# Kernel optimization log

Hardware: AMD Instinct MI355X
Metric: run time of the kernel (lower is better)

The kernel has to match this reference:

```python
import jax, jax.numpy as jnp
import numpy as np

N, L, S = 512, 1024, 32   # batch, latent dim, spatial (S*S == L)
F = 32 * S * S            # flattened encoder conv features (last conv = 32 ch)
H = 512                   # hidden width of latent MLP heads


def _lrelu(x):
    return jnp.where(x >= 0, x, 0.01 * x)


def _bn(x):
    # BatchNorm2d in training mode, gamma=1, beta=0 (default init)
    m = x.mean((0, 2, 3), keepdims=True)
    v = x.var((0, 2, 3), keepdims=True)
    return (x - m) * jax.lax.rsqrt(v + 1e-5)


def _conv(x, w, b):
    y = jax.lax.conv_general_dilated(x, w, (1, 1), 'SAME',
                                     dimension_numbers=('NCHW', 'OIHW', 'NCHW'))
    return y + b[None, :, None, None]


def _block(x, w, b):
    return _lrelu(_bn(_conv(x, w, b)))


def setup_inputs() -> dict:
    key = jax.random.key(0)
    ks = jax.random.split(key, 16)
    r = lambda k, s, sc: jax.random.normal(k, s, jnp.float32) * sc
    return {
        'x': r(ks[0], (N, 1, S, S), 1.0),
        'eps_c': r(ks[1], (N, L), 1.0),
        'eps_s': r(ks[2], (N, L), 1.0),
        'enc_cw1': r(ks[3], (2, 32, 1, 3, 3), 0.1),   'enc_cb1': jnp.zeros((2, 32)),
        'enc_cw2': r(ks[4], (2, 64, 32, 3, 3), 0.05), 'enc_cb2': jnp.zeros((2, 64)),
        'enc_cw3': r(ks[5], (2, 32, 64, 3, 3), 0.05), 'enc_cb3': jnp.zeros((2, 32)),
        'enc_muW1': r(ks[6], (2, H, F), 0.005), 'enc_muB1': jnp.zeros((2, H)),
        'enc_muW2': r(ks[7], (2, L, H), 0.02),  'enc_muB2': jnp.zeros((2, L)),
        'enc_vaW1': r(ks[8], (2, H, F), 0.005), 'enc_vaB1': jnp.zeros((2, H)),
        'enc_vaW2': r(ks[9], (2, L, H), 0.02),  'enc_vaB2': jnp.zeros((2, L)),
        'dec_cw1': r(ks[10], (2, 32, 1, 3, 3), 0.1),   'dec_cb1': jnp.zeros((2, 32)),
        'dec_cw2': r(ks[11], (2, 64, 32, 3, 3), 0.05), 'dec_cb2': jnp.zeros((2, 64)),
        'dec_cw3': r(ks[12], (2, 1, 64, 3, 3), 0.05),  'dec_cb3': jnp.zeros((2, 1)),
    }


def reference(x, eps_c, eps_s,
              enc_cw1, enc_cb1, enc_cw2, enc_cb2, enc_cw3, enc_cb3,
              enc_muW1, enc_muB1, enc_muW2, enc_muB2,
              enc_vaW1, enc_vaB1, enc_vaW2, enc_vaB2,
              dec_cw1, dec_cb1, dec_cw2, dec_cb2, dec_cw3, dec_cb3):
    def encode(i):
        h = _block(x, enc_cw1[i], enc_cb1[i])
        h = _block(h, enc_cw2[i], enc_cb2[i])
        h = _block(h, enc_cw3[i], enc_cb3[i])
        f = h.reshape(N, -1)                                   # [N, F]
        mu = _lrelu(_lrelu(f @ enc_muW1[i].T + enc_muB1[i]) @ enc_muW2[i].T + enc_muB2[i])
        lv = _lrelu(_lrelu(f @ enc_vaW1[i].T + enc_vaB1[i]) @ enc_vaW2[i].T + enc_vaB2[i])
        return mu, lv                                          # each [N, L]

    def decode(z, i):
        h = z.reshape(N, 1, S, S)
        h = _block(h, dec_cw1[i], dec_cb1[i])
        h = _block(h, dec_cw2[i], dec_cb2[i])
        h = _block(h, dec_cw3[i], dec_cb3[i])
        return h.reshape(N, 1, S, S)

    class_mu, class_logvar = encode(0)
    style_mu, style_logvar = encode(1)

    # precision-weighted product-of-experts group evidence (vectorized)
    precision = jnp.exp(-style_logvar)                  # 1/var, [N, L]
    group_var = 1.0 / precision.sum(0)                  # [L]
    group_mu = (style_mu * precision).sum(0) * group_var  # [L]
    group_logvar = jnp.log(group_var)

    # reparameterize
    z_c = eps_c * jnp.exp(0.5 * class_logvar) + class_mu          # [N, L]
    z_s = eps_s * jnp.exp(0.5 * group_logvar)[None] + group_mu[None]  # [N, L]

    output_c = decode(z_c, 0)
    output_s = jax.nn.relu(decode(z_s, 1))
    output = output_c * output_s                        # [N, 1, S, S]

    kl1 = -0.5 * jnp.sum(1.0 + class_logvar) + 0.5 * (
        jnp.sum(class_mu ** 2) + jnp.sum(jnp.exp(class_logvar) ** 2))
    kl2 = -0.5 * jnp.sum(1.0 + group_logvar) + 0.5 * (
        jnp.sum(group_mu ** 2) + jnp.sum(jnp.exp(group_logvar) ** 2))
    recon = (jnp.exp(x) - jnp.exp(output)) ** 2
    loss = -kl1 + kl2 + recon                           # [N, 1, S, S]
    return loss, output
```

## Files before the change

### kernel.cpp

```cpp
#include <hip/hip_runtime.h>

constexpr int N_   = 512;
constexpr int PIX  = 1024;
constexpr int L_   = 1024;
constexpr int F_   = 32768;
constexpr int H_   = 512;
constexpr float IC_ = 1.0f / (float)(512 * 1024);

__device__ __forceinline__ float lrelu(float t) { return t >= 0.f ? t : 0.01f * t; }

using frag  = __attribute__((ext_vector_type(8))) short;
using f32x4 = __attribute__((ext_vector_type(4))) float;
using s4    = __attribute__((ext_vector_type(4))) short;

#define BAR() do {                                              \
    asm volatile("s_waitcnt lgkmcnt(0)" ::: "memory");          \
    __builtin_amdgcn_s_barrier();                               \
    asm volatile("" ::: "memory");                              \
} while (0)

__device__ __forceinline__ void split_bf16(float v, short& hi, short& lo) {
    const unsigned b = __float_as_uint(v);
    hi = (short)(b >> 16);
    const float hf = __uint_as_float(b & 0xFFFF0000u);
    lo = (short)(__float_as_uint(v - hf) >> 16);
}

__device__ __forceinline__ frag ld2(const short* p) {
    union { frag f; struct { unsigned long long a, b; } u; } x;
    x.u.a = *(const unsigned long long*)(p);
    x.u.b = *(const unsigned long long*)(p + 4);
    return x.f;
}

__global__ __launch_bounds__(256) void wsplit6_kernel(
    const float* __restrict__ w0, const float* __restrict__ w1,
    const float* __restrict__ w2, const float* __restrict__ w3,
    const float* __restrict__ w4, const float* __restrict__ w5,
    short* __restrict__ hi, short* __restrict__ lo)
{
    const int layer = blockIdx.y;
    const float* W = layer == 0 ? w0 : layer == 1 ? w1 : layer == 2 ? w2 :
                     layer == 3 ? w3 : layer == 4 ? w4 : w5;
    const int CIN  = (layer == 1 || layer == 3) ? 64 : 32;
    const int NCOT = (layer == 1 || layer == 3) ? 2 : 4;
    const int idx = blockIdx.x * 256 + threadIdx.x;
    const int j    = idx & 7;
    const int lane = (idx >> 3) & 63;
    const int q    = lane >> 4, lm = lane & 15;
    const int blk  = idx >> 9;
    const int cot  = blk % NCOT;
    const int rest = blk / NCOT;
    const int pos  = rest % 9;
    const int cc   = rest / 9;
    const int co = cot * 16 + lm;
    const int ci = cc * 32 + q * 8 + j;
    short h, l;
    split_bf16(W[((size_t)co * CIN + ci) * 9 + pos], h, l);
    hi[layer * 18432 + idx] = h;
    lo[layer * 18432 + idx] = l;
}

template<int CIN, int COUT, bool BN_IN>
__global__ __launch_bounds__(512) void conv_mfma(
    const float* __restrict__ in, const short* __restrict__ wh,
    const short* __restrict__ wl, const float* __restrict__ bias,
    float* __restrict__ out, const float* __restrict__ stats_in,
    float* __restrict__ stats_out)
{
    constexpr int NCOT  = COUT / 16;
    constexpr int NCOT2 = NCOT / 2;
    constexpr int NCH   = CIN / 32;
    constexpr int STR  = 36;
    constexpr int PLsh = 340 * STR;
    __shared__ __align__(16) short hiL[PLsh];
    __shared__ __align__(16) short loL[PLsh];
    __shared__ float red[2 * COUT];
    __shared__ float bnm[64], bni[64];
    const int tid  = threadIdx.x;
    const int n    = blockIdx.x >> 2;
    const int y0   = (blockIdx.x & 3) << 3;
    const int lane = tid & 63;
    const int wv   = tid >> 6;
    const int pgrp = wv & 3;
    const int cotg = wv >> 2;
    const int lm   = lane & 15;
    const int q    = lane >> 4;

    if (tid < 2 * COUT) red[tid] = 0.f;
    if (BN_IN && tid < CIN) {
        const float m  = stats_in[tid] * IC_;
        const float qq = stats_in[CIN + tid] * IC_;
        bnm[tid] = m;
        bni[tid] = rsqrtf(qq - m * m + 1e-5f);
    }
    __syncthreads();

    f32x4 acc[NCOT2][4];
#pragma unroll
    for (int t = 0; t < NCOT2; ++t)
#pragma unroll
        for (int pt = 0; pt < 4; ++pt) acc[t][pt] = {0.f, 0.f, 0.f, 0.f};

    const int rs0 = tid / 34, cs0 = tid % 34;
    const int gr0 = y0 - 1 + rs0, gc0 = cs0 - 1;
    const bool act = tid < 340;
    const bool ok0 = act && ((unsigned)gr0 < 32u) && ((unsigned)gc0 < 32u);
    const int  po0 = gr0 * 32 + gc0;

    const float* inb = in + ((size_t)n * CIN << 10);

    frag ahA[NCOT2], alA[NCOT2], ahB[NCOT2], alB[NCOT2];

    auto LDW = [&](frag (&dh)[NCOT2], frag (&dl)[NCOT2], int posAbs) {
#pragma unroll
        for (int t = 0; t < NCOT2; ++t) {
            const int cot = cotg * NCOT2 + t;
            const size_t wb = (size_t)((posAbs * NCOT + cot) * 512 + lane * 8);
            dh[t] = *(const frag*)&wh[wb];
            dl[t] = *(const frag*)&wl[wb];
        }
    };

    auto COMPUTE = [&](int pos, frag (&fh)[NCOT2], frag (&fl)[NCOT2]) {
        const int ky = pos / 3, kx = pos - ky * 3;
        __builtin_amdgcn_s_setprio(1);
#pragma unroll
        for (int pt = 0; pt < 4; ++pt) {
            const int ptile = pgrp * 4 + pt;
            const int row = ptile >> 1;
            const int col = ((ptile & 1) << 4) + lm;
            const int loff = ((row + ky) * 34 + col + kx) * STR + q * 8;
            const frag bh = ld2(&hiL[loff]);
            const frag bl = ld2(&loL[loff]);
#pragma unroll
            for (int t = 0; t < NCOT2; ++t) {
                acc[t][pt] = __builtin_amdgcn_mfma_f32_16x16x32_bf16(
                    fh[t], bh, acc[t][pt], 0, 0, 0);
                acc[t][pt] = __builtin_amdgcn_mfma_f32_16x16x32_bf16(
                    fh[t], bl, acc[t][pt], 0, 0, 0);
                acc[t][pt] = __builtin_amdgcn_mfma_f32_16x16x32_bf16(
                    fl[t], bh, acc[t][pt], 0, 0, 0);
            }
        }
        __builtin_amdgcn_s_setprio(0);
    };

#pragma unroll 1
    for (int cc = 0; cc < NCH; ++cc) {
        if (cc) BAR();

        LDW(ahA, alA, cc * 9 + 0);

#pragma unroll 1
        for (int cb = 0; cb < 32; cb += 16) {
            float v0r[16];
#pragma unroll
            for (int u = 0; u < 16; ++u) {
                const int cg = cc * 32 + cb + u;
                v0r[u] = ok0 ? inb[((size_t)cg << 10) + po0] : 0.f;
            }
            if (act) {
#pragma unroll
                for (int u4 = 0; u4 < 16; u4 += 4) {
                    s4 h0v, l0v;
#pragma unroll
                    for (int e = 0; e < 4; ++e) {
                        const int ci = cb + u4 + e;
                        const int cg = cc * 32 + ci;
                        float v0 = v0r[u4 + e];
                        if (BN_IN && ok0) v0 = lrelu((v0 - bnm[cg]) * bni[cg]);
                        short h, l;
                        split_bf16(v0, h, l);
                        h0v[e] = h; l0v[e] = l;
                    }
                    *(s4*)&hiL[tid * STR + cb + u4] = h0v;
                    *(s4*)&loL[tid * STR + cb + u4] = l0v;
                }
            }
        }
        BAR();

#pragma unroll 1
        for (int pos = 0; pos < 8; pos += 2) {
            LDW(ahB, alB, cc * 9 + pos + 1);
            COMPUTE(pos, ahA, alA);
            LDW(ahA, alA, cc * 9 + pos + 2);
            COMPUTE(pos + 1, ahB, alB);
        }
        COMPUTE(8, ahA, alA);
    }

    float* ob = out + ((size_t)n * COUT << 10);
#pragma unroll
    for (int t = 0; t < NCOT2; ++t) {
#pragma unroll
        for (int r = 0; r < 4; ++r) {
            const int co = (cotg * NCOT2 + t) * 16 + q * 4 + r;
            const float b = bias[co];
            float s = 0.f, sq = 0.f;
#pragma unroll
            for (int pt = 0; pt < 4; ++pt) {
                const int ptile = pgrp * 4 + pt;
                const float v = acc[t][pt][r] + b;
                ob[((size_t)co << 10) + (y0 << 5) + (ptile << 4) + lm] = v;
                s += v; sq += v * v;
            }
#pragma unroll
            for (int off = 8; off > 0; off >>= 1) {
                s  += __shfl_down(s, off, 64);
                sq += __shfl_down(sq, off, 64);
            }
            if (lm == 0) {
                atomicAdd(&red[co], s);
                atomicAdd(&red[COUT + co], sq);
            }
        }
    }
    __syncthreads();
    if (tid < 2 * COUT) atomicAdd(&stats_out[tid], red[tid]);
}

template<int CIN, int COPB, bool BN_IN>
__global__ __launch_bounds__(256) void conv3x3(
    const float* __restrict__ in, const float* __restrict__ w,
    const float* __restrict__ bias, float* __restrict__ out,
    const float* __restrict__ stats_in, float* __restrict__ stats_out,
    int Cout)
{
    constexpr int CT = (CIN < 4) ? CIN : 4;
    __shared__ float tile[CT * PIX];
    __shared__ float red[2 * COPB];
    const int groups = Cout / COPB;
    const int n   = blockIdx.x / groups;
    const int co0 = (blockIdx.x % groups) * COPB;
    const int tid = threadIdx.x;
    const int x   = tid & 31;
    const int y0  = (tid >> 5) * 4;

    float acc[COPB][4];
#pragma unroll
    for (int c = 0; c < COPB; ++c)
#pragma unroll
        for (int j = 0; j < 4; ++j) acc[c][j] = 0.f;

    const float* inbase = in + (size_t)n * CIN * PIX;

#pragma unroll 1
    for (int s0 = 0; s0 < CIN; s0 += CT) {
        __syncthreads();
#pragma unroll
        for (int s = 0; s < CT; ++s) {
            float4 v = ((const float4*)(inbase + (size_t)(s0 + s) * PIX))[tid];
            if (BN_IN) {
                const int c = s0 + s;
                const float m   = stats_in[c] * IC_;
                const float q   = stats_in[CIN + c] * IC_;
                const float inv = rsqrtf(q - m * m + 1e-5f);
                v.x = lrelu((v.x - m) * inv);
                v.y = lrelu((v.y - m) * inv);
                v.z = lrelu((v.z - m) * inv);
                v.w = lrelu((v.w - m) * inv);
            }
            ((float4*)tile)[s * 256 + tid] = v;
        }
        __syncthreads();
#pragma unroll 2
        for (int s = 0; s < CT; ++s) {
            const int ci = s0 + s;
            const float* tp = tile + s * PIX;
            float r[6][3];
#pragma unroll
            for (int ry = 0; ry < 6; ++ry) {
                const int yy = y0 + ry - 1;
                const bool yok = (unsigned)yy < 32u;
#pragma unroll
                for (int cx = 0; cx < 3; ++cx) {
                    const int xx = x + cx - 1;
                    const bool ok = yok && ((unsigned)xx < 32u);
                    r[ry][cx] = ok ? tp[yy * 32 + xx] : 0.f;
                }
            }
#pragma unroll
            for (int c = 0; c < COPB; ++c) {
                const float* wp = w + ((size_t)(co0 + c) * CIN + ci) * 9;
#pragma unroll
                for (int ky = 0; ky < 3; ++ky)
#pragma unroll
                    for (int kx = 0; kx < 3; ++kx) {
                        const float wv = wp[ky * 3 + kx];
#pragma unroll
                        for (int j = 0; j < 4; ++j)
                            acc[c][j] += r[ky + j][kx] * wv;
                    }
            }
        }
    }

    if (tid < 2 * COPB) red[tid] = 0.f;
    __syncthreads();
#pragma unroll
    for (int c = 0; c < COPB; ++c) {
        const float b = bias[co0 + c];
        float* ob = out + (((size_t)n * Cout + co0 + c) << 10);
        float s = 0.f, q = 0.f;
#pragma unroll
        for (int j = 0; j < 4; ++j) {
            const float v = acc[c][j] + b;
            ob[(y0 + j) * 32 + x] = v;
            s += v; q += v * v;
        }
#pragma unroll
        for (int off = 32; off > 0; off >>= 1) {
            s += __shfl_down(s, off, 64);
            q += __shfl_down(q, off, 64);
        }
        if ((tid & 63) == 0) {
            atomicAdd(&red[c], s);
            atomicAdd(&red[COPB + c], q);
        }
    }
    __syncthreads();
    if (tid < COPB)
        atomicAdd(&stats_out[co0 + tid], red[tid]);
    else if (tid < 2 * COPB)
        atomicAdd(&stats_out[Cout + co0 + tid - COPB], red[tid]);
}

template<int MODE>
__global__ __launch_bounds__(256) void gemm_mfma(
    const float* __restrict__ A0, const float* __restrict__ A1,
    const float* __restrict__ B0, const float* __restrict__ B1,
    float* __restrict__ C0, float* __restrict__ C1,
    int K, int Nh, int kchunk, int xph,
    const float* __restrict__ bnstats, int Cin,
    const float* __restrict__ ba0, const float* __restrict__ ba1)
{
    __shared__ short AhL[8192], AlL[8192], BhL[8192], BlL[8192];
    const int tid  = threadIdx.x;
    const int head = blockIdx.x / xph;
    const int n0   = (blockIdx.x % xph) * 128;
    const int m0   = blockIdx.y * 128;
    const float* A = head ? A1 : A0;
    const float* B = head ? B1 : B0;
    float*       C = head ? C1 : C0;
    const float* BA = head ? ba1 : ba0;
    const int k0 = blockIdx.z * kchunk;

    const int lane = tid & 63;
    const int wv   = tid >> 6;
    const int wm   = wv & 1;
    const int wn   = wv >> 1;
    const int lm   = lane & 15;
    const int q    = lane >> 4;

    const int srow = tid >> 1;
    const int smt  = srow >> 4;
    const int slm  = srow & 15;
    const int sq0  = (tid & 1) * 2;
    const int ks   = (tid & 1) * 16;

    float bnm0 = 0.f, bni0 = 1.f, bnm1 = 0.f, bni1 = 1.f;
    if (MODE == 1) {
        const int c0 = k0 >> 10;
        bnm0 = bnstats[c0] * IC_;
        const float q0 = bnstats[Cin + c0] * IC_;
        bni0 = rsqrtf(q0 - bnm0 * bnm0 + 1e-5f);
        const int c1 = (c0 + 1 < Cin) ? c0 + 1 : c0;
        bnm1 = bnstats[c1] * IC_;
        const float q1 = bnstats[Cin + c1] * IC_;
        bni1 = rsqrtf(q1 - bnm1 * bnm1 + 1e-5f);
    }

    f32x4 acc[4][4];
#pragma unroll
    for (int i = 0; i < 4; ++i)
#pragma unroll
        for (int j = 0; j < 4; ++j) acc[i][j] = {0.f, 0.f, 0.f, 0.f};

    auto cv8 = [](float4 u, float4 w2, frag& h, frag& l) {
        const float v[8] = {u.x, u.y, u.z, u.w, w2.x, w2.y, w2.z, w2.w};
#pragma unroll
        for (int e = 0; e < 8; ++e) {
            short hh, ll;
            split_bf16(v[e], hh, ll);
            h[e] = hh; l[e] = ll;
        }
    };

    float4 a4[4], b4[4];
    auto LOADAB = [&](int kb) {
        const float* Ap = A + (size_t)(m0 + srow) * K + kb + ks;
        const float* Bp = B + (size_t)(n0 + srow) * K + kb + ks;
#pragma unroll
        for (int g = 0; g < 4; ++g) a4[g] = ((const float4*)Ap)[g];
#pragma unroll
        for (int g = 0; g < 4; ++g) b4[g] = ((const float4*)Bp)[g];
    };

    const int o0 = ((smt * 4 + sq0) * 16 + slm) * 8;
    const int o1 = ((smt * 4 + sq0 + 1) * 16 + slm) * 8;

    auto STAGE = [&](int s) {
        if (MODE == 1) {
            const int sel = s >> 5;
            const float m   = sel ? bnm1 : bnm0;
            const float inv = sel ? bni1 : bni0;
#pragma unroll
            for (int g = 0; g < 4; ++g) {
                a4[g].x = lrelu((a4[g].x - m) * inv);
                a4[g].y = lrelu((a4[g].y - m) * inv);
                a4[g].z = lrelu((a4[g].z - m) * inv);
                a4[g].w = lrelu((a4[g].w - m) * inv);
            }
        }
        if (MODE == 2) {
            const float* bp = BA + k0 + s * 32 + ks;
#pragma unroll
            for (int g = 0; g < 4; ++g) {
                const float4 bv = ((const float4*)bp)[g];
                a4[g].x = lrelu(a4[g].x + bv.x);
                a4[g].y = lrelu(a4[g].y + bv.y);
                a4[g].z = lrelu(a4[g].z + bv.z);
                a4[g].w = lrelu(a4[g].w + bv.w);
            }
        }
        frag ah0, al0, ah1, al1, bh0, bl0, bh1, bl1;
        cv8(a4[0], a4[1], ah0, al0);
        cv8(a4[2], a4[3], ah1, al1);
        cv8(b4[0], b4[1], bh0, bl0);
        cv8(b4[2], b4[3], bh1, bl1);
        const int pb = (s & 1) << 12;
        *(frag*)&AhL[pb + o0] = ah0;  *(frag*)&AhL[pb + o1] = ah1;
        *(frag*)&AlL[pb + o0] = al0;  *(frag*)&AlL[pb + o1] = al1;
        *(frag*)&BhL[pb + o0] = bh0;  *(frag*)&BhL[pb + o1] = bh1;
        *(frag*)&BlL[pb + o0] = bl0;  *(frag*)&BlL[pb + o1] = bl1;
    };

    auto MMA = [&](int s) {
        const int pb = (s & 1) << 12;
        frag fah[4], fal[4], fbh[4], fbl[4];
#pragma unroll
        for (int t = 0; t < 4; ++t) {
            const int oa = pb + (((wm * 4 + t) * 4 + q) * 16 + lm) * 8;
            const int ob = pb + (((wn * 4 + t) * 4 + q) * 16 + lm) * 8;
            fah[t] = *(const frag*)&AhL[oa];
            fal[t] = *(const frag*)&AlL[oa];
            fbh[t] = *(const frag*)&BhL[ob];
            fbl[t] = *(const frag*)&BlL[ob];
        }
        __builtin_amdgcn_s_setprio(1);
#pragma unroll
        for (int i = 0; i < 4; ++i)
#pragma unroll
            for (int j = 0; j < 4; ++j) {
                acc[i][j] = __builtin_amdgcn_mfma_f32_16x16x32_bf16(
                    fah[i], fbh[j], acc[i][j], 0, 0, 0);
                acc[i][j] = __builtin_amdgcn_mfma_f32_16x16x32_bf16(
                    fah[i], fbl[j], acc[i][j], 0, 0, 0);
                acc[i][j] = __builtin_amdgcn_mfma_f32_16x16x32_bf16(
                    fal[i], fbh[j], acc[i][j], 0, 0, 0);
            }
        __builtin_amdgcn_s_setprio(0);
    };

    const int T = kchunk >> 5;

    LOADAB(k0);
    STAGE(0);
    LOADAB(k0 + 32);
    BAR();

#pragma unroll 1
    for (int s = 1; s < T; ++s) {
        MMA(s - 1);
        STAGE(s);
        if (s + 1 < T) LOADAB(k0 + (s + 1) * 32);
        BAR();
    }
    MMA(T - 1);

#pragma unroll
    for (int i = 0; i < 4; ++i) {
        const int m = m0 + wm * 64 + i * 16 + q * 4;
#pragma unroll
        for (int j = 0; j < 4; ++j) {
            const int n = n0 + wn * 64 + j * 16 + lm;
            float* cp = C + (size_t)m * Nh + n;
#pragma unroll
            for (int r = 0; r < 4; ++r)
                atomicAdd(cp + (size_t)r * Nh, acc[i][j][r]);
        }
    }
}

__device__ __forceinline__ void block_reduce_atomic(float t, float* target)
{
#pragma unroll
    for (int off = 32; off > 0; off >>= 1) t += __shfl_down(t, off, 64);
    __shared__ float lt[4];
    const int wave = threadIdx.x >> 6, lane = threadIdx.x & 63;
    if (lane == 0) lt[wave] = t;
    __syncthreads();
    if (threadIdx.x == 0) atomicAdd(target, lt[0] + lt[1] + lt[2] + lt[3]);
}

__global__ __launch_bounds__(256) void poe_kernel(
    const float* __restrict__ mu1, const float* __restrict__ lv1,
    const float* __restrict__ bmu, const float* __restrict__ blv,
    float* __restrict__ gmu, float* __restrict__ glv, float* __restrict__ kl)
{
    const int l = blockIdx.x * 256 + threadIdx.x;
    const float bm = bmu[l], bl = blv[l];
    float sp = 0.f, sm = 0.f;
    for (int n = 0; n < N_; ++n) {
        const float lv = lrelu(lv1[(size_t)n * L_ + l] + bl);
        const float p  = expf(-lv);
        sp += p;
        sm += lrelu(mu1[(size_t)n * L_ + l] + bm) * p;
    }
    const float gv = 1.f / sp;
    const float gm = sm * gv;
    const float gl = -logf(sp);
    gmu[l] = gm;
    glv[l] = gl;
    const float t = -0.5f * (1.f + gl) + 0.5f * (gm * gm + gv * gv);
    block_reduce_atomic(t, &kl[1]);
}

__global__ __launch_bounds__(256) void reparam_kernel(
    const float* __restrict__ mu0, const float* __restrict__ lv0,
    const float* __restrict__ bmu, const float* __restrict__ blv,
    const float* __restrict__ eps_c, const float* __restrict__ eps_s,
    const float* __restrict__ gmu, const float* __restrict__ glv,
    float* __restrict__ zc, float* __restrict__ zs, float* __restrict__ kl)
{
    const int idx = blockIdx.x * 256 + threadIdx.x;
    const int l = idx & (L_ - 1);
    const float m  = lrelu(mu0[idx] + bmu[l]);
    const float lv = lrelu(lv0[idx] + blv[l]);
    zc[idx] = eps_c[idx] * expf(0.5f * lv) + m;
    zs[idx] = eps_s[idx] * expf(0.5f * glv[l]) + gmu[l];
    const float e = expf(lv);
    const float t = -0.5f * (1.f + lv) + 0.5f * (m * m + e * e);
    block_reduce_atomic(t, &kl[0]);
}

__global__ __launch_bounds__(256) void final_kernel(
    const float* __restrict__ x, const float* __restrict__ oc,
    const float* __restrict__ os, const float* __restrict__ stC,
    const float* __restrict__ stS, const float* __restrict__ kl,
    float* __restrict__ out)
{
    const int idx = blockIdx.x * 256 + threadIdx.x;
    const float mc = stC[0] * IC_, qc = stC[1] * IC_;
    const float ivc = rsqrtf(qc - mc * mc + 1e-5f);
    const float ms = stS[0] * IC_, qs = stS[1] * IC_;
    const float ivs = rsqrtf(qs - ms * ms + 1e-5f);
    const float tc = lrelu((oc[idx] - mc) * ivc);
    const float ts = fmaxf((os[idx] - ms) * ivs, 0.f);
    const float o = tc * ts;
    const float d = expf(x[idx]) - expf(o);
    out[idx]            = -kl[0] + kl[1] + d * d;
    out[N_ * PIX + idx] = o;
}

extern "C" void kernel_launch(void* const* d_in, const int* in_sizes, int n_in,
                              void* d_out, int out_size, void* d_ws, size_t ws_size,
                              hipStream_t stream)
{
    const float* x        = (const float*)d_in[0];
    const float* eps_c    = (const float*)d_in[1];
    const float* eps_s    = (const float*)d_in[2];
    const float* enc_cw1  = (const float*)d_in[3];
    const float* enc_cb1  = (const float*)d_in[4];
    const float* enc_cw2  = (const float*)d_in[5];
    const float* enc_cb2  = (const float*)d_in[6];
    const float* enc_cw3  = (const float*)d_in[7];
    const float* enc_cb3  = (const float*)d_in[8];
    const float* enc_muW1 = (const float*)d_in[9];
    const float* enc_muB1 = (const float*)d_in[10];
    const float* enc_muW2 = (const float*)d_in[11];
    const float* enc_muB2 = (const float*)d_in[12];
    const float* enc_vaW1 = (const float*)d_in[13];
    const float* enc_vaB1 = (const float*)d_in[14];
    const float* enc_vaW2 = (const float*)d_in[15];
    const float* enc_vaB2 = (const float*)d_in[16];
    const float* dec_cw1  = (const float*)d_in[17];
    const float* dec_cb1  = (const float*)d_in[18];
    const float* dec_cw2  = (const float*)d_in[19];
    const float* dec_cb2  = (const float*)d_in[20];
    const float* dec_cw3  = (const float*)d_in[21];
    const float* dec_cb3  = (const float*)d_in[22];
    float* out = (float*)d_out;

    float* ws   = (float*)d_ws;
    float* bufA = ws;
    float* bufB = bufA + (size_t)N_ * 64 * PIX;
    float* h1   = bufB + (size_t)N_ * 32 * PIX;
    float* h2   = h1 + N_ * H_;
    float* mu0  = h2 + N_ * H_;
    float* lv0  = mu0 + N_ * L_;
    float* mu1  = lv0 + N_ * L_;
    float* lv1  = mu1 + N_ * L_;
    float* zc   = lv1 + N_ * L_;
    float* zs   = zc + N_ * L_;
    float* oc   = zs + N_ * L_;
    float* os   = oc + N_ * L_;
    float* gmu  = os + N_ * L_;
    float* glv  = gmu + L_;
    float* stats = glv + L_;
    float* kl   = stats + 12 * 128;
    short* wsh  = (short*)(kl + 4);
    short* wsl  = wsh + 6 * 18432;

    auto st  = [&](int s) { return stats + 128 * s; };
    auto whp = [&](int layer) { return wsh + layer * 18432; };
    auto wlp = [&](int layer) { return wsl + layer * 18432; };

    hipMemsetAsync(stats, 0, (12 * 128 + 4) * sizeof(float), stream);

    wsplit6_kernel<<<dim3(72, 6), 256, 0, stream>>>(
        enc_cw2, enc_cw3, enc_cw2 + 64 * 32 * 9, enc_cw3 + 32 * 64 * 9,
        dec_cw2, dec_cw2 + 64 * 32 * 9, wsh, wsl);

    for (int i = 0; i < 2; ++i) {
        const float* cw1 = enc_cw1 + (size_t)i * 32 * 9;
        const float* cb1 = enc_cb1 + (size_t)i * 32;
        const float* cb2 = enc_cb2 + (size_t)i * 64;
        const float* cb3 = enc_cb3 + (size_t)i * 32;

        conv3x3<1, 16, false><<<N_ * 2, 256, 0, stream>>>(
            x, cw1, cb1, bufB, nullptr, st(i * 3 + 0), 32);
        conv_mfma<32, 64, true><<<N_ * 4, 512, 0, stream>>>(
            bufB, whp(i * 2), wlp(i * 2), cb2, bufA, st(i * 3 + 0), st(i * 3 + 1));
        conv_mfma<64, 32, true><<<N_ * 4, 512, 0, stream>>>(
            bufA, whp(i * 2 + 1), wlp(i * 2 + 1), cb3, bufB, st(i * 3 + 1), st(i * 3 + 2));

        const float* W1m = enc_muW1 + (size_t)i * H_ * F_;
        const float* B1m = enc_muB1 + (size_t)i * H_;
        const float* W2m = enc_muW2 + (size_t)i * L_ * H_;
        const float* W1v = enc_vaW1 + (size_t)i * H_ * F_;
        const float* B1v = enc_vaB1 + (size_t)i * H_;
        const float* W2v = enc_vaW2 + (size_t)i * L_ * H_;
        float* mu_i = (i == 0) ? mu0 : mu1;
        float* lv_i = (i == 0) ? lv0 : lv1;

        hipMemsetAsync(h1, 0, (size_t)2 * N_ * H_ * sizeof(float), stream);
        gemm_mfma<1><<<dim3(8, 4, 16), 256, 0, stream>>>(
            bufB, bufB, W1m, W1v, h1, h2, F_, H_, 2048, 4,
            st(i * 3 + 2), 32, nullptr, nullptr);

        hipMemsetAsync(mu_i, 0, (size_t)2 * N_ * L_ * sizeof(float), stream);
        gemm_mfma<2><<<dim3(16, 4, 4), 256, 0, stream>>>(
            h1, h2, W2m, W2v, mu_i, lv_i, H_, L_, 128, 8,
            nullptr, 0, B1m, B1v);
    }

    poe_kernel<<<L_ / 256, 256, 0, stream>>>(
        mu1, lv1, enc_muB2 + L_, enc_vaB2 + L_, gmu, glv, kl);
    reparam_kernel<<<(N_ * L_) / 256, 256, 0, stream>>>(
        mu0, lv0, enc_muB2, enc_vaB2, eps_c, eps_s, gmu, glv, zc, zs, kl);

    for (int i = 0; i < 2; ++i) {
        const float* cw1 = dec_cw1 + (size_t)i * 32 * 9;
        const float* cb1 = dec_cb1 + (size_t)i * 32;
        const float* cb2 = dec_cb2 + (size_t)i * 64;
        const float* cw3 = dec_cw3 + (size_t)i * 64 * 9;
        const float* cb3 = dec_cb3 + (size_t)i * 1;
        const float* zi = (i == 0) ? zc : zs;
        float* oi = (i == 0) ? oc : os;

        conv3x3<1, 16, false><<<N_ * 2, 256, 0, stream>>>(
            zi, cw1, cb1, bufB, nullptr, st(6 + i * 3 + 0), 32);
        conv_mfma<32, 64, true><<<N_ * 4, 512, 0, stream>>>(
            bufB, whp(4 + i), wlp(4 + i), cb2, bufA, st(6 + i * 3 + 0), st(6 + i * 3 + 1));
        conv3x3<64, 1, true><<<N_, 256, 0, stream>>>(
            bufA, cw3, cb3, oi, st(6 + i * 3 + 1), st(6 + i * 3 + 2), 1);
    }

    final_kernel<<<(N_ * PIX) / 256, 256, 0, stream>>>(
        x, oc, os, st(8), st(11), kl, out);
}
```

Measured before the change: 1.365 ms.

## Load GEMM tiles straight to LDS as fp32 and split to bf16 after reading

The MFMA GEMM now fills double-buffered fp32 LDS tiles with global_load_lds (16-byte, XOR-swizzled) instead of loading through registers and writing pre-split bf16 hi/lo tiles. The BN/bias activation and the bf16 hi/lo split move into the MMA stage, applied to fragments read from LDS. The aim is to cut register staging and VALU work between the global loads and the LDS stores, and to overlap the next tile's loads with the current tile's MFMAs. In exchange, conversion now sits on the critical path before the MFMAs, and there is a full vmcnt wait plus a barrier every stage.

```diff
diff --git a/kernel.cpp b/kernel.cpp
--- a/kernel.cpp
+++ b/kernel.cpp
@@ -31,6 +31,12 @@
     x.u.a = *(const unsigned long long*)(p);
     x.u.b = *(const unsigned long long*)(p + 4);
     return x.f;
+}
+
+__device__ __forceinline__ void gll16(const float* g, float* l) {
+    __builtin_amdgcn_global_load_lds(
+        (const __attribute__((address_space(1))) void*)g,
+        (__attribute__((address_space(3))) void*)l, 16, 0, 0);
 }
 
 __global__ __launch_bounds__(256) void wsplit6_kernel(
@@ -336,7 +342,8 @@
     const float* __restrict__ bnstats, int Cin,
     const float* __restrict__ ba0, const float* __restrict__ ba1)
 {
-    __shared__ short AhL[8192], AlL[8192], BhL[8192], BlL[8192];
+    __shared__ __align__(16) float AfL[2 * 4096];
+    __shared__ __align__(16) float BfL[2 * 4096];
     const int tid  = threadIdx.x;
     const int head = blockIdx.x / xph;
     const int n0   = (blockIdx.x % xph) * 128;
@@ -354,11 +361,8 @@
     const int lm   = lane & 15;
     const int q    = lane >> 4;
 
-    const int srow = tid >> 1;
-    const int smt  = srow >> 4;
-    const int slm  = srow & 15;
-    const int sq0  = (tid & 1) * 2;
-    const int ks   = (tid & 1) * 16;
+    const int lrow = lane >> 3;
+    const int lpk  = ((lane & 7) ^ lrow) << 2;
 
     float bnm0 = 0.f, bni0 = 1.f, bnm1 = 0.f, bni1 = 1.f;
     if (MODE == 1) {
@@ -378,76 +382,56 @@
 #pragma unroll
         for (int j = 0; j < 4; ++j) acc[i][j] = {0.f, 0.f, 0.f, 0.f};
 
-    auto cv8 = [](float4 u, float4 w2, frag& h, frag& l) {
-        const float v[8] = {u.x, u.y, u.z, u.w, w2.x, w2.y, w2.z, w2.w};
-#pragma unroll
-        for (int e = 0; e < 8; ++e) {
-            short hh, ll;
-            split_bf16(v[e], hh, ll);
-            h[e] = hh; l[e] = ll;
+    auto ISSUE = [&](int s, int kb) {
+        float* lba = &AfL[(s & 1) << 12];
+        float* lbb = &BfL[(s & 1) << 12];
+#pragma unroll
+        for (int j = 0; j < 4; ++j) {
+            const int c = wv * 4 + j;
+            const int row = (c << 3) + lrow;
+            gll16(A + (size_t)(m0 + row) * K + kb + lpk, lba + (c << 8));
+            gll16(B + (size_t)(n0 + row) * K + kb + lpk, lbb + (c << 8));
         }
     };
 
-    float4 a4[4], b4[4];
-    auto LOADAB = [&](int kb) {
-        const float* Ap = A + (size_t)(m0 + srow) * K + kb + ks;
-        const float* Bp = B + (size_t)(n0 + srow) * K + kb + ks;
-#pragma unroll
-        for (int g = 0; g < 4; ++g) a4[g] = ((const float4*)Ap)[g];
-#pragma unroll
-        for (int g = 0; g < 4; ++g) b4[g] = ((const float4*)Bp)[g];
-    };
-
-    const int o0 = ((smt * 4 + sq0) * 16 + slm) * 8;
-    const int o1 = ((smt * 4 + sq0 + 1) * 16 + slm) * 8;
-
-    auto STAGE = [&](int s) {
+    auto MMA = [&](int s, int kb) {
+        const float* Ap = &AfL[(s & 1) << 12];
+        const float* Bp = &BfL[(s & 1) << 12];
+        float bm = 0.f, bi = 1.f;
         if (MODE == 1) {
-            const int sel = s >> 5;
-            const float m   = sel ? bnm1 : bnm0;
-            const float inv = sel ? bni1 : bni0;
-#pragma unroll
-            for (int g = 0; g < 4; ++g) {
-                a4[g].x = lrelu((a4[g].x - m) * inv);
-                a4[g].y = lrelu((a4[g].y - m) * inv);
-                a4[g].z = lrelu((a4[g].z - m) * inv);
-                a4[g].w = lrelu((a4[g].w - m) * inv);
-            }
-        }
+            const int sel = s & 32;
+            bm = sel ? bnm1 : bnm0;
+            bi = sel ? bni1 : bni0;
+        }
+        float bv[8];
         if (MODE == 2) {
-            const float* bp = BA + k0 + s * 32 + ks;
-#pragma unroll
-            for (int g = 0; g < 4; ++g) {
-                const float4 bv = ((const float4*)bp)[g];
-                a4[g].x = lrelu(a4[g].x + bv.x);
-                a4[g].y = lrelu(a4[g].y + bv.y);
-                a4[g].z = lrelu(a4[g].z + bv.z);
-                a4[g].w = lrelu(a4[g].w + bv.w);
-            }
-        }
-        frag ah0, al0, ah1, al1, bh0, bl0, bh1, bl1;
-        cv8(a4[0], a4[1], ah0, al0);
-        cv8(a4[2], a4[3], ah1, al1);
-        cv8(b4[0], b4[1], bh0, bl0);
-        cv8(b4[2], b4[3], bh1, bl1);
-        const int pb = (s & 1) << 12;
-        *(frag*)&AhL[pb + o0] = ah0;  *(frag*)&AhL[pb + o1] = ah1;
-        *(frag*)&AlL[pb + o0] = al0;  *(frag*)&AlL[pb + o1] = al1;
-        *(frag*)&BhL[pb + o0] = bh0;  *(frag*)&BhL[pb + o1] = bh1;
-        *(frag*)&BlL[pb + o0] = bl0;  *(frag*)&BlL[pb + o1] = bl1;
-    };
-
-    auto MMA = [&](int s) {
-        const int pb = (s & 1) << 12;
+            const float* bp = BA + kb + q * 8;
+            *(float4*)&bv[0] = ((const float4*)bp)[0];
+            *(float4*)&bv[4] = ((const float4*)bp)[1];
+        }
         frag fah[4], fal[4], fbh[4], fbl[4];
 #pragma unroll
         for (int t = 0; t < 4; ++t) {
-            const int oa = pb + (((wm * 4 + t) * 4 + q) * 16 + lm) * 8;
-            const int ob = pb + (((wn * 4 + t) * 4 + q) * 16 + lm) * 8;
-            fah[t] = *(const frag*)&AhL[oa];
-            fal[t] = *(const frag*)&AlL[oa];
-            fbh[t] = *(const frag*)&BhL[ob];
-            fbl[t] = *(const frag*)&BlL[ob];
+            const int ra = wm * 64 + t * 16 + lm;
+            const int rb = wn * 64 + t * 16 + lm;
+            const int ma = ra & 7, mb = rb & 7;
+            float va[8], vb[8];
+            *(float4*)&va[0] = *(const float4*)&Ap[ra * 32 + ((( q << 1)      ^ ma) << 2)];
+            *(float4*)&va[4] = *(const float4*)&Ap[ra * 32 + ((((q << 1) | 1) ^ ma) << 2)];
+            *(float4*)&vb[0] = *(const float4*)&Bp[rb * 32 + ((( q << 1)      ^ mb) << 2)];
+            *(float4*)&vb[4] = *(const float4*)&Bp[rb * 32 + ((((q << 1) | 1) ^ mb) << 2)];
+#pragma unroll
+            for (int e = 0; e < 8; ++e) {
+                float v = va[e];
+                if (MODE == 1) v = lrelu((v - bm) * bi);
+                if (MODE == 2) v = lrelu(v + bv[e]);
+                short hh, ll;
+                split_bf16(v, hh, ll);
+                fah[t][e] = hh; fal[t][e] = ll;
+                short h2, l2;
+                split_bf16(vb[e], h2, l2);
+                fbh[t][e] = h2; fbl[t][e] = l2;
+            }
         }
         __builtin_amdgcn_s_setprio(1);
 #pragma unroll
@@ -466,19 +450,17 @@
 
     const int T = kchunk >> 5;
 
-    LOADAB(k0);
-    STAGE(0);
-    LOADAB(k0 + 32);
-    BAR();
+    ISSUE(0, k0);
+    asm volatile("s_waitcnt vmcnt(0)" ::: "memory");
+    __syncthreads();
 
 #pragma unroll 1
-    for (int s = 1; s < T; ++s) {
-        MMA(s - 1);
-        STAGE(s);
-        if (s + 1 < T) LOADAB(k0 + (s + 1) * 32);
+    for (int s = 0; s < T; ++s) {
+        if (s + 1 < T) ISSUE(s + 1, k0 + (s + 1) * 32);
+        MMA(s, k0 + s * 32);
+        asm volatile("s_waitcnt vmcnt(0)" ::: "memory");
         BAR();
     }
-    MMA(T - 1);
 
 #pragma unroll
     for (int i = 0; i < 4; ++i) {
```

New measurement: 1.418 ms. +3.9%, slower.
